# Kernel tuning notes

Hardware: AMD Instinct MI355X
Metric: run time of the kernel (lower is better)

## Reference

```python
import jax, jax.numpy as jnp
import numpy as np

D_K = 128


def setup_inputs() -> dict:
    key = jax.random.key(0)
    k1, k2, k3, k4 = jax.random.split(key, 4)
    return {
        "value_in": jax.random.normal(k1, (4, 2048, 1024), dtype=jnp.float32),
        "w_q": jax.random.normal(k2, (1024, D_K), dtype=jnp.float32),
        "w_k": jax.random.normal(k3, (1024, D_K), dtype=jnp.float32),
        "w_v": jax.random.normal(k4, (1024, 128), dtype=jnp.float32),
    }


def reference(value_in, w_q, w_k, w_v):
    # Projections: [B,S,d_model] @ [d_model,d] -> [B,S,d]
    q = jnp.einsum('bsm,mk->bsk', value_in, w_q)
    k = jnp.einsum('bsm,mk->bsk', value_in, w_k)
    v = jnp.einsum('bsm,mv->bsv', value_in, w_v)
    # Scores [B,S,S], scaled by sqrt(d_k)
    scores = jnp.einsum('bqk,bsk->bqs', q, k) / jnp.sqrt(jnp.float32(D_K))
    S = scores.shape[-1]
    # Causal mask: keep lower triangle (q_idx >= k_idx), -inf elsewhere
    causal = jnp.tril(jnp.ones((S, S), dtype=bool))
    scores = jnp.where(causal, scores, -jnp.inf)
    # NOTE: softmax over the QUERY axis (dim=-2), not the key axis
    attention = jax.nn.softmax(scores, axis=-2)
    out = jnp.einsum('bqs,bsv->bqv', attention, v)
    return out, attention
```

## Files before the change

### kernel.cpp

```cpp
#include <hip/hip_runtime.h>
#include <math.h>

constexpr int B  = 4;
constexpr int S  = 2048;
constexpr int DM = 1024;
constexpr int DK = 128;
constexpr int BS = B * S;
constexpr int NSP = 8;

static constexpr float SCALE = 0.08838834764831845f;

typedef __attribute__((ext_vector_type(8))) short bf16x8;
typedef __attribute__((ext_vector_type(4))) float f32x4;
typedef __attribute__((ext_vector_type(8))) unsigned short u16x8;

__device__ __forceinline__ unsigned short f2bf(float x) {
  unsigned u = __float_as_uint(x);
  unsigned r = (u + 0x7FFFu + ((u >> 16) & 1u)) >> 16;
  return (unsigned short)r;
}
__device__ __forceinline__ float bf2f(unsigned short h) {
  return __uint_as_float(((unsigned)h) << 16);
}

__device__ __forceinline__ void gload16(const void* g, void* l) {
  __builtin_amdgcn_global_load_lds(
      (const __attribute__((address_space(1))) void*)g,
      (__attribute__((address_space(3))) void*)l, 16, 0, 0);
}

__global__ __launch_bounds__(256) void cvt_hilo(
    const float* __restrict__ x, unsigned short* __restrict__ hi,
    unsigned short* __restrict__ lo)
{
  const size_t idx = (size_t)blockIdx.x * 256 + threadIdx.x;
  const float4 v = ((const float4*)x)[idx];
  ushort4 h, l;
  h.x = f2bf(v.x); l.x = f2bf(v.x - bf2f(h.x));
  h.y = f2bf(v.y); l.y = f2bf(v.y - bf2f(h.y));
  h.z = f2bf(v.z); l.z = f2bf(v.z - bf2f(h.z));
  h.w = f2bf(v.w); l.w = f2bf(v.w - bf2f(h.w));
  ((ushort4*)hi)[idx] = h;
  ((ushort4*)lo)[idx] = l;
}

__global__ void cvtw_kernel(const float* __restrict__ wq, const float* __restrict__ wk,
                            const float* __restrict__ wv,
                            unsigned short* __restrict__ Wth, unsigned short* __restrict__ Wtl)
{
  const int n = blockIdx.x;
  const int p = n >> 7, c = n & 127;
  const float* w = (p == 0) ? wq : (p == 1) ? wk : wv;
  for (int k = threadIdx.x; k < DM; k += 256) {
    const float x = w[(size_t)k * DK + c];
    const unsigned short h = f2bf(x);
    Wth[(size_t)n * DM + k] = h;
    Wtl[(size_t)n * DM + k] = f2bf(x - bf2f(h));
  }
}

__global__ __launch_bounds__(256) void proj_mfma(
    const unsigned short* __restrict__ Ah, const unsigned short* __restrict__ Al,
    const unsigned short* __restrict__ Wh, const unsigned short* __restrict__ Wl,
    unsigned short* __restrict__ qh, unsigned short* __restrict__ ql,
    unsigned short* __restrict__ kh, unsigned short* __restrict__ kl,
    float* __restrict__ vtmp)
{
  __shared__ unsigned short Ash[2][64 * 64];
  __shared__ unsigned short Wsh[2][64 * 64];

  const int r0 = blockIdx.x * 64;
  const int n0 = blockIdx.y * 64;
  const int t  = threadIdx.x;
  const int l  = t & 63, w = t >> 6;
  const int wm = w >> 1, wn = w & 1;
  const int fr = l & 15, kg = l >> 4;

  f32x4 acc[2][2] = {};

  for (int k0 = 0; k0 < DM; k0 += 64) {
    #pragma unroll
    for (int i = 0; i < 2; ++i) {
      const int flat = t + i * 256;
      const int row = flat >> 3, sg = flat & 7;
      const int sgs = sg ^ (row & 7);
      const size_t ga = (size_t)(r0 + row) * DM + k0 + sgs * 8;
      const size_t gw = (size_t)(n0 + row) * DM + k0 + sgs * 8;
      gload16(Ah + ga, &Ash[0][flat * 8]);
      gload16(Al + ga, &Ash[1][flat * 8]);
      gload16(Wh + gw, &Wsh[0][flat * 8]);
      gload16(Wl + gw, &Wsh[1][flat * 8]);
    }
    __syncthreads();

    #pragma unroll
    for (int kk = 0; kk < 2; ++kk) {
      bf16x8 ah[2], al[2], bh[2], bl[2];
      #pragma unroll
      for (int im = 0; im < 2; ++im) {
        const int row = wm * 32 + im * 16 + fr;
        const int off = row * 64 + ((kk * 4 + kg) ^ (row & 7)) * 8;
        ah[im] = *(const bf16x8*)&Ash[0][off];
        al[im] = *(const bf16x8*)&Ash[1][off];
      }
      #pragma unroll
      for (int in = 0; in < 2; ++in) {
        const int row = wn * 32 + in * 16 + fr;
        const int off = row * 64 + ((kk * 4 + kg) ^ (row & 7)) * 8;
        bh[in] = *(const bf16x8*)&Wsh[0][off];
        bl[in] = *(const bf16x8*)&Wsh[1][off];
      }
      #pragma unroll
      for (int im = 0; im < 2; ++im)
        #pragma unroll
        for (int in = 0; in < 2; ++in) {
          acc[im][in] = __builtin_amdgcn_mfma_f32_16x16x32_bf16(ah[im], bh[in], acc[im][in], 0, 0, 0);
          acc[im][in] = __builtin_amdgcn_mfma_f32_16x16x32_bf16(ah[im], bl[in], acc[im][in], 0, 0, 0);
          acc[im][in] = __builtin_amdgcn_mfma_f32_16x16x32_bf16(al[im], bh[in], acc[im][in], 0, 0, 0);
        }
    }
    __syncthreads();
  }

  const int crow = kg * 4;
  #pragma unroll
  for (int im = 0; im < 2; ++im)
    #pragma unroll
    for (int in = 0; in < 2; ++in) {
      const int n = n0 + wn * 32 + in * 16 + fr;
      const int p = n >> 7, c = n & 127;
      #pragma unroll
      for (int r = 0; r < 4; ++r) {
        const int m = r0 + wm * 32 + im * 16 + crow + r;
        const float val = acc[im][in][r];
        if (p == 2) {
          vtmp[(size_t)m * DK + c] = val;
        } else {
          const unsigned short h = f2bf(val);
          const unsigned short lo2 = f2bf(val - bf2f(h));
          unsigned short* hd = p ? kh : qh;
          unsigned short* ld = p ? kl : ql;
          hd[(size_t)m * DK + c] = h;
          ld[(size_t)m * DK + c] = lo2;
        }
      }
    }
}

__global__ __launch_bounds__(256) void cvtv_kernel(
    const float* __restrict__ v, unsigned short* __restrict__ vTh,
    unsigned short* __restrict__ vTl)
{
  const int s0 = blockIdx.x * 64, d0 = blockIdx.y * 64, b = blockIdx.z;
  __shared__ float Ts[64][65];
  const int t = threadIdx.x;
  const int r = t >> 4, c4 = (t & 15) * 4;
  #pragma unroll
  for (int rr = 0; rr < 4; ++rr) {
    const int sl = r + 16 * rr;
    *(float4*)&Ts[sl][c4] =
        *(const float4*)&v[((size_t)b * S + s0 + sl) * DK + d0 + c4];
  }
  __syncthreads();
  const int dl = t >> 2, sq = (t & 3) * 16;
  unsigned short hbuf[16], lbuf[16];
  #pragma unroll
  for (int j = 0; j < 16; ++j) {
    const float val = Ts[sq + j][dl];
    hbuf[j] = f2bf(val);
    lbuf[j] = f2bf(val - bf2f(hbuf[j]));
  }
  const size_t o = (size_t)b * DK * S + (size_t)(d0 + dl) * S + s0 + sq;
  #pragma unroll
  for (int half = 0; half < 2; ++half) {
    *(u16x8*)&vTh[o + half * 8] = *(u16x8*)&hbuf[half * 8];
    *(u16x8*)&vTl[o + half * 8] = *(u16x8*)&lbuf[half * 8];
  }
}

__global__ __launch_bounds__(256) void stats_mfma(
    const unsigned short* __restrict__ qh, const unsigned short* __restrict__ ql,
    const unsigned short* __restrict__ kh, const unsigned short* __restrict__ kl,
    float* __restrict__ pm, float* __restrict__ ps)
{
  const int sp = blockIdx.x, qt = blockIdx.y, b = blockIdx.z;
  if (sp > qt) return;
  const int q0 = qt * 64;

  __shared__ unsigned short Bsh[64 * 128], Bsl[64 * 128];
  __shared__ float SmL[64 * 2], SeL[64 * 2];

  const int t = threadIdx.x;
  const int l = t & 63, w = t >> 6;
  const int wm = w >> 1, wn = w & 1;
  const int fr = l & 15, kg = l >> 4;

  #pragma unroll
  for (int i = 0; i < 4; ++i) {
    const int flat = t + i * 256;
    const int row = flat >> 4, sg = flat & 15;
    const int sgs = sg ^ (row & 7);
    const size_t gq = (size_t)(b * S + q0 + row) * DK + sgs * 8;
    gload16(qh + gq, &Bsh[flat * 8]);
    gload16(ql + gq, &Bsl[flat * 8]);
  }
  __syncthreads();
  bf16x8 qfh[2][4], qfl[2][4];
  #pragma unroll
  for (int im = 0; im < 2; ++im)
    #pragma unroll
    for (int ks = 0; ks < 4; ++ks) {
      const int row = wm * 32 + im * 16 + fr;
      const int off = row * 128 + ((ks * 4 + kg) ^ (row & 7)) * 8;
      qfh[im][ks] = *(const bf16x8*)&Bsh[off];
      qfl[im][ks] = *(const bf16x8*)&Bsl[off];
    }
  __syncthreads();

  for (int st = sp; st <= qt; st += NSP) {
    const int s0 = st * 64;

    #pragma unroll
    for (int i = 0; i < 4; ++i) {
      const int flat = t + i * 256;
      const int row = flat >> 4, sg = flat & 15;
      const int sgs = sg ^ (row & 7);
      const size_t gk = (size_t)(b * S + s0 + row) * DK + sgs * 8;
      gload16(kh + gk, &Bsh[flat * 8]);
      gload16(kl + gk, &Bsl[flat * 8]);
    }
    __syncthreads();

    f32x4 acc[2][2] = {};
    #pragma unroll
    for (int ks = 0; ks < 4; ++ks) {
      bf16x8 bh[2], bl[2];
      #pragma unroll
      for (int in = 0; in < 2; ++in) {
        const int row = wn * 32 + in * 16 + fr;
        const int off = row * 128 + ((ks * 4 + kg) ^ (row & 7)) * 8;
        bh[in] = *(const bf16x8*)&Bsh[off];
        bl[in] = *(const bf16x8*)&Bsl[off];
      }
      #pragma unroll
      for (int im = 0; im < 2; ++im)
        #pragma unroll
        for (int in = 0; in < 2; ++in) {
          acc[im][in] = __builtin_amdgcn_mfma_f32_16x16x32_bf16(qfh[im][ks], bh[in], acc[im][in], 0, 0, 0);
          acc[im][in] = __builtin_amdgcn_mfma_f32_16x16x32_bf16(qfh[im][ks], bl[in], acc[im][in], 0, 0, 0);
          acc[im][in] = __builtin_amdgcn_mfma_f32_16x16x32_bf16(qfl[im][ks], bh[in], acc[im][in], 0, 0, 0);
        }
    }

    const bool diag = (st == qt);
    float Sm_[2], Se_[2];
    #pragma unroll
    for (int in = 0; in < 2; ++in) {
      const int scol = s0 + wn * 32 + in * 16 + fr;
      float m8 = -INFINITY;
      #pragma unroll
      for (int im = 0; im < 2; ++im)
        #pragma unroll
        for (int r = 0; r < 4; ++r) {
          const int q = q0 + wm * 32 + im * 16 + kg * 4 + r;
          if (!diag || q >= scol) m8 = fmaxf(m8, acc[im][in][r] * SCALE);
        }
      float e8 = 0.f;
      if (m8 > -INFINITY) {
        #pragma unroll
        for (int im = 0; im < 2; ++im)
          #pragma unroll
          for (int r = 0; r < 4; ++r) {
            const int q = q0 + wm * 32 + im * 16 + kg * 4 + r;
            if (!diag || q >= scol) e8 += __expf(acc[im][in][r] * SCALE - m8);
          }
      }
      #pragma unroll
      for (int off = 16; off <= 32; off <<= 1) {
        const float om = __shfl_xor(m8, off);
        const float oe = __shfl_xor(e8, off);
        const float nm = fmaxf(m8, om);
        float ne = 0.f;
        if (m8 > -INFINITY) ne += e8 * __expf(m8 - nm);
        if (om > -INFINITY) ne += oe * __expf(om - nm);
        m8 = nm; e8 = ne;
      }
      Sm_[in] = m8; Se_[in] = e8;
    }
    if (l < 16) {
      #pragma unroll
      for (int in = 0; in < 2; ++in) {
        const int col = wn * 32 + in * 16 + l;
        SmL[col * 2 + wm] = Sm_[in];
        SeL[col * 2 + wm] = Se_[in];
      }
    }
    __syncthreads();
    if (t < 64) {
      const float m0 = SmL[t * 2 + 0], m1 = SmL[t * 2 + 1];
      const float nm = fmaxf(m0, m1);
      float ne = 0.f;
      if (m0 > -INFINITY) ne += SeL[t * 2 + 0] * __expf(m0 - nm);
      if (m1 > -INFINITY) ne += SeL[t * 2 + 1] * __expf(m1 - nm);
      const size_t o = ((size_t)(b * 32 + qt)) * S + s0 + t;
      pm[o] = nm;
      ps[o] = ne;
    }
    __syncthreads();
  }
}

__global__ void colcombine_kernel(const float* __restrict__ pm, const float* __restrict__ ps,
                                  float* __restrict__ cm, float* __restrict__ cinv)
{
  const int s = blockIdx.x * 256 + threadIdx.x;
  const int b = blockIdx.y;
  const int ch0 = s >> 6;
  float m = -INFINITY;
  for (int ch = ch0; ch < 32; ++ch)
    m = fmaxf(m, pm[((size_t)(b * 32 + ch)) * S + s]);
  float sum = 0.f;
  for (int ch = ch0; ch < 32; ++ch) {
    const size_t i = ((size_t)(b * 32 + ch)) * S + s;
    sum += ps[i] * __expf(pm[i] - m);
  }
  cm[(size_t)b * S + s]   = m;
  cinv[(size_t)b * S + s] = 1.f / sum;
}

__global__ void zero_out_kernel(float* __restrict__ out)
{
  const size_t idx = (size_t)blockIdx.x * 256 + threadIdx.x;
  ((float4*)out)[idx] = float4{0.f, 0.f, 0.f, 0.f};
}

__global__ __launch_bounds__(256) void fused_pv(
    const unsigned short* __restrict__ qh, const unsigned short* __restrict__ ql,
    const unsigned short* __restrict__ kh, const unsigned short* __restrict__ kl,
    const unsigned short* __restrict__ vTh, const unsigned short* __restrict__ vTl,
    const float* __restrict__ cm, const float* __restrict__ cinv,
    float* __restrict__ att, float* __restrict__ out)
{
  const int sp = blockIdx.x, qt = blockIdx.y, b = blockIdx.z;
  if (sp > qt) return;
  const int q0 = qt * 64;
  float* attb = att + (size_t)b * S * S;
  const unsigned short* vth = vTh + (size_t)b * DK * S;
  const unsigned short* vtl = vTl + (size_t)b * DK * S;

  __shared__ unsigned short Ksh[64 * 128], Ksl[64 * 128];
  __shared__ unsigned short Vsh[128 * 64], Vsl[128 * 64];
  __shared__ unsigned short Psh[64 * 64];

  const int t = threadIdx.x;
  const int l = t & 63, w = t >> 6;
  const int wm = w >> 1, wn = w & 1;
  const int fr = l & 15, kg = l >> 4;

  #pragma unroll
  for (int i = 0; i < 4; ++i) {
    const int flat = t + i * 256;
    const int row = flat >> 4, sg = flat & 15;
    const int sgs = sg ^ (row & 7);
    const size_t gq = (size_t)(b * S + q0 + row) * DK + sgs * 8;
    gload16(qh + gq, &Ksh[flat * 8]);
    gload16(ql + gq, &Ksl[flat * 8]);
  }
  __syncthreads();
  bf16x8 qfh[2][4], qfl[2][4];
  #pragma unroll
  for (int im = 0; im < 2; ++im)
    #pragma unroll
    for (int ks = 0; ks < 4; ++ks) {
      const int row = wm * 32 + im * 16 + fr;
      const int off = row * 128 + ((ks * 4 + kg) ^ (row & 7)) * 8;
      qfh[im][ks] = *(const bf16x8*)&Ksh[off];
      qfl[im][ks] = *(const bf16x8*)&Ksl[off];
    }
  __syncthreads();

  f32x4 acc[8] = {};

  for (int st = sp; st <= qt; st += NSP) {
    const int s0 = st * 64;

    #pragma unroll
    for (int i = 0; i < 4; ++i) {
      const int flat = t + i * 256;
      const int row = flat >> 4, sg = flat & 15;
      const int sgs = sg ^ (row & 7);
      const size_t gk = (size_t)(b * S + s0 + row) * DK + sgs * 8;
      gload16(kh + gk, &Ksh[flat * 8]);
      gload16(kl + gk, &Ksl[flat * 8]);
    }
    #pragma unroll
    for (int i = 0; i < 4; ++i) {
      const int flat = t + i * 256;
      const int row = flat >> 3, sg = flat & 7;
      const int sgs = sg ^ (row & 7);
      const size_t gv = (size_t)row * S + s0 + sgs * 8;
      gload16(vth + gv, &Vsh[flat * 8]);
      gload16(vtl + gv, &Vsl[flat * 8]);
    }
    __syncthreads();

    f32x4 sacc[2][2] = {};
    #pragma unroll
    for (int ks = 0; ks < 4; ++ks) {
      bf16x8 bh[2], bl[2];
      #pragma unroll
      for (int in = 0; in < 2; ++in) {
        const int row = wn * 32 + in * 16 + fr;
        const int off = row * 128 + ((ks * 4 + kg) ^ (row & 7)) * 8;
        bh[in] = *(const bf16x8*)&Ksh[off];
        bl[in] = *(const bf16x8*)&Ksl[off];
      }
      #pragma unroll
      for (int im = 0; im < 2; ++im)
        #pragma unroll
        for (int in = 0; in < 2; ++in) {
          sacc[im][in] = __builtin_amdgcn_mfma_f32_16x16x32_bf16(qfh[im][ks], bh[in], sacc[im][in], 0, 0, 0);
          sacc[im][in] = __builtin_amdgcn_mfma_f32_16x16x32_bf16(qfh[im][ks], bl[in], sacc[im][in], 0, 0, 0);
          sacc[im][in] = __builtin_amdgcn_mfma_f32_16x16x32_bf16(qfl[im][ks], bh[in], sacc[im][in], 0, 0, 0);
        }
    }

    const bool diag = (st == qt);
    float xv[2][2][4];
    #pragma unroll
    for (int in = 0; in < 2; ++in) {
      const int sloc = wn * 32 + in * 16 + fr;
      const int scol = s0 + sloc;
      const float m   = cm[(size_t)b * S + scol];
      const float inv = cinv[(size_t)b * S + scol];
      #pragma unroll
      for (int im = 0; im < 2; ++im) {
        #pragma unroll
        for (int r = 0; r < 4; ++r) {
          const int qloc = wm * 32 + im * 16 + kg * 4 + r;
          const bool live = !diag || (q0 + qloc >= scol);
          const float x = live ? __expf(sacc[im][in][r] * SCALE - m) * inv : 0.f;
          xv[im][in][r] = x;
          const int idx = qloc * 64 + (((sloc >> 3) ^ (qloc & 7)) * 8 + (sloc & 7));
          Psh[idx] = f2bf(x);
        }
      }
    }

    if (st < qt) {
      const f32x4 z = {0.f, 0.f, 0.f, 0.f};
      #pragma unroll
      for (int i = 0; i < 4; ++i) {
        const int flat = t + i * 256;
        const int row = flat >> 4, c4 = (flat & 15) * 4;
        __builtin_nontemporal_store(z, (f32x4*)&attb[(size_t)(s0 + row) * S + q0 + c4]);
      }
    }

    #pragma unroll
    for (int im = 0; im < 2; ++im)
      #pragma unroll
      for (int in = 0; in < 2; ++in) {
        const int sloc = wn * 32 + in * 16 + fr;
        #pragma unroll
        for (int r = 0; r < 4; ++r) {
          const int qloc = wm * 32 + im * 16 + kg * 4 + r;
          __builtin_nontemporal_store(xv[im][in][r],
                                      &attb[(size_t)(q0 + qloc) * S + s0 + sloc]);
        }
      }
    __syncthreads();

    #pragma unroll
    for (int ks2 = 0; ks2 < 2; ++ks2) {
      const int arow = w * 16 + fr;
      const int aoff = arow * 64 + ((ks2 * 4 + kg) ^ (arow & 7)) * 8;
      const bf16x8 a = *(const bf16x8*)&Psh[aoff];
      #pragma unroll
      for (int in = 0; in < 8; ++in) {
        const int brow = in * 16 + fr;
        const int boff = brow * 64 + ((ks2 * 4 + kg) ^ (brow & 7)) * 8;
        const bf16x8 b_h = *(const bf16x8*)&Vsh[boff];
        const bf16x8 b_l = *(const bf16x8*)&Vsl[boff];
        acc[in] = __builtin_amdgcn_mfma_f32_16x16x32_bf16(a, b_h, acc[in], 0, 0, 0);
        acc[in] = __builtin_amdgcn_mfma_f32_16x16x32_bf16(a, b_l, acc[in], 0, 0, 0);
      }
    }
    __syncthreads();
  }

  #pragma unroll
  for (int in = 0; in < 8; ++in) {
    #pragma unroll
    for (int r = 0; r < 4; ++r) {
      const int q = q0 + w * 16 + kg * 4 + r;
      const int d = in * 16 + fr;
      atomicAdd(&out[((size_t)b * S + q) * DK + d], acc[in][r]);
    }
  }
}

extern "C" void kernel_launch(void* const* d_in, const int* in_sizes, int n_in,
                              void* d_out, int out_size, void* d_ws, size_t ws_size,
                              hipStream_t stream)
{
  const float* vin = (const float*)d_in[0];
  const float* wq  = (const float*)d_in[1];
  const float* wk  = (const float*)d_in[2];
  const float* wv  = (const float*)d_in[3];

  float* out = (float*)d_out;
  float* att = out + (size_t)B * S * DK;

  unsigned short* Ah  = (unsigned short*)att;
  unsigned short* Al  = Ah  + (size_t)BS * DM;
  unsigned short* Wth = Al  + (size_t)BS * DM;
  unsigned short* Wtl = Wth + (size_t)384 * DM;

  constexpr size_t NE = (size_t)BS * DK;
  unsigned short* qh  = (unsigned short*)d_ws;
  unsigned short* ql  = qh  + NE;
  unsigned short* kh  = ql  + NE;
  unsigned short* kl  = kh  + NE;
  unsigned short* vTh = kl  + NE;
  unsigned short* vTl = vTh + NE;
  float* vtmp = (float*)(vTl + NE);
  float* pm   = vtmp;
  float* ps   = pm + 32ull * B * S;
  float* cm   = ps + 32ull * B * S;
  float* cinv = cm + (size_t)B * S;

  cvt_hilo         <<<dim3(BS * DM / 1024),  256, 0, stream>>>(vin, Ah, Al);
  cvtw_kernel      <<<dim3(384),             256, 0, stream>>>(wq, wk, wv, Wth, Wtl);
  proj_mfma        <<<dim3(128, 6),          256, 0, stream>>>(Ah, Al, Wth, Wtl,
                                                               qh, ql, kh, kl, vtmp);
  cvtv_kernel      <<<dim3(S / 64, 2, B),    256, 0, stream>>>(vtmp, vTh, vTl);
  zero_out_kernel  <<<dim3(BS * DK / 1024),  256, 0, stream>>>(out);
  stats_mfma       <<<dim3(NSP, 32, B),      256, 0, stream>>>(qh, ql, kh, kl, pm, ps);
  colcombine_kernel<<<dim3(S / 256, B),      256, 0, stream>>>(pm, ps, cm, cinv);
  fused_pv         <<<dim3(NSP, 32, B),      256, 0, stream>>>(qh, ql, kh, kl, vTh, vTl,
                                                               cm, cinv, att, out);
}
```

Before: 117.8 us.

## Defer attention-tile stores to next iteration to overlap with K/V loads

Stores of the attention tile and its mirrored zero tile are moved from right after the softmax into the start of the next iteration. There they are issued after the next K/V global loads and before the barrier, with an epilogue that flushes the final tile. The intent is to overlap the large global write traffic with load latency and MFMA work instead of serialising it between barriers. A trailing __syncthreads in the stats kernel loop is also dropped. This keeps xv live across iterations, which raises register pressure, and relies on the removed barrier being unnecessary.

After: 115.5 us. About the same (-1.9%).

```diff
diff --git a/kernel.cpp b/kernel.cpp
--- a/kernel.cpp
+++ b/kernel.cpp
@@ -306,7 +306,6 @@
       pm[o] = nm;
       ps[o] = ne;
     }
-    __syncthreads();
   }
 }
 
@@ -380,6 +379,9 @@
   __syncthreads();
 
   f32x4 acc[8] = {};
+  float xv[2][2][4];
+  int prev_s0 = -1;
+  int prev_mirror = 0;
 
   for (int st = sp; st <= qt; st += NSP) {
     const int s0 = st * 64;
@@ -402,6 +404,30 @@
       gload16(vth + gv, &Vsh[flat * 8]);
       gload16(vtl + gv, &Vsl[flat * 8]);
     }
+
+    if (prev_s0 >= 0) {
+      if (prev_mirror) {
+        const f32x4 z = {0.f, 0.f, 0.f, 0.f};
+        #pragma unroll
+        for (int i = 0; i < 4; ++i) {
+          const int flat = t + i * 256;
+          const int row = flat >> 4, c4 = (flat & 15) * 4;
+          __builtin_nontemporal_store(z, (f32x4*)&attb[(size_t)(prev_s0 + row) * S + q0 + c4]);
+        }
+      }
+      #pragma unroll
+      for (int im = 0; im < 2; ++im)
+        #pragma unroll
+        for (int in = 0; in < 2; ++in) {
+          const int sloc = wn * 32 + in * 16 + fr;
+          #pragma unroll
+          for (int r = 0; r < 4; ++r) {
+            const int qloc = wm * 32 + im * 16 + kg * 4 + r;
+            __builtin_nontemporal_store(xv[im][in][r],
+                                        &attb[(size_t)(q0 + qloc) * S + prev_s0 + sloc]);
+          }
+        }
+    }
     __syncthreads();
 
     f32x4 sacc[2][2] = {};
@@ -426,7 +452,6 @@
     }
 
     const bool diag = (st == qt);
-    float xv[2][2][4];
     #pragma unroll
     for (int in = 0; in < 2; ++in) {
       const int sloc = wn * 32 + in * 16 + fr;
@@ -446,29 +471,6 @@
         }
       }
     }
-
-    if (st < qt) {
-      const f32x4 z = {0.f, 0.f, 0.f, 0.f};
-      #pragma unroll
-      for (int i = 0; i < 4; ++i) {
-        const int flat = t + i * 256;
-        const int row = flat >> 4, c4 = (flat & 15) * 4;
-        __builtin_nontemporal_store(z, (f32x4*)&attb[(size_t)(s0 + row) * S + q0 + c4]);
-      }
-    }
-
-    #pragma unroll
-    for (int im = 0; im < 2; ++im)
-      #pragma unroll
-      for (int in = 0; in < 2; ++in) {
-        const int sloc = wn * 32 + in * 16 + fr;
-        #pragma unroll
-        for (int r = 0; r < 4; ++r) {
-          const int qloc = wm * 32 + im * 16 + kg * 4 + r;
-          __builtin_nontemporal_store(xv[im][in][r],
-                                      &attb[(size_t)(q0 + qloc) * S + s0 + sloc]);
-        }
-      }
     __syncthreads();
 
     #pragma unroll
@@ -487,6 +489,33 @@
       }
     }
     __syncthreads();
+
+    prev_s0 = s0;
+    prev_mirror = (st < qt) ? 1 : 0;
+  }
+
+  if (prev_s0 >= 0) {
+    if (prev_mirror) {
+      const f32x4 z = {0.f, 0.f, 0.f, 0.f};
+      #pragma unroll
+      for (int i = 0; i < 4; ++i) {
+        const int flat = t + i * 256;
+        const int row = flat >> 4, c4 = (flat & 15) * 4;
+        __builtin_nontemporal_store(z, (f32x4*)&attb[(size_t)(prev_s0 + row) * S + q0 + c4]);
+      }
+    }
+    #pragma unroll
+    for (int im = 0; im < 2; ++im)
+      #pragma unroll
+      for (int in = 0; in < 2; ++in) {
+        const int sloc = wn * 32 + in * 16 + fr;
+        #pragma unroll
+        for (int r = 0; r < 4; ++r) {
+          const int qloc = wm * 32 + im * 16 + kg * 4 + r;
+          __builtin_nontemporal_store(xv[im][in][r],
+                                      &attb[(size_t)(q0 + qloc) * S + prev_s0 + sloc]);
+        }
+      }
   }
 
   #pragma unroll
```

## Double the query tile to 128 rows with 512-thread blocks in stats and PV

Applied to the files above, without the earlier changes.

The stats and fused PV kernels now cover 128 query rows per block using 8 waves instead of 4. Each loaded K and V tile is reused across twice as many queries, which halves global and LDS traffic per output, and the partial-stat chunk count drops from 32 to 16. Attention probabilities are now stored inline as they are computed rather than buffered in registers first. The trade-offs are fewer blocks with a coarser diagonal-masking granularity, higher LDS use per block, and one barrier removed from the stats loop.

Measured after the change: 116.2 us. Within noise of the previous version (-1.3%).

```diff
diff --git a/kernel.cpp b/kernel.cpp
--- a/kernel.cpp
+++ b/kernel.cpp
@@ -7,6 +7,7 @@
 constexpr int DK = 128;
 constexpr int BS = B * S;
 constexpr int NSP = 8;
+constexpr int QT  = 16;
 
 static constexpr float SCALE = 0.08838834764831845f;
 
@@ -178,17 +179,18 @@
   }
 }
 
-__global__ __launch_bounds__(256) void stats_mfma(
+__global__ __launch_bounds__(512) void stats_mfma(
     const unsigned short* __restrict__ qh, const unsigned short* __restrict__ ql,
     const unsigned short* __restrict__ kh, const unsigned short* __restrict__ kl,
     float* __restrict__ pm, float* __restrict__ ps)
 {
   const int sp = blockIdx.x, qt = blockIdx.y, b = blockIdx.z;
-  if (sp > qt) return;
-  const int q0 = qt * 64;
-
-  __shared__ unsigned short Bsh[64 * 128], Bsl[64 * 128];
-  __shared__ float SmL[64 * 2], SeL[64 * 2];
+  const int stmax = 2 * qt + 1;
+  if (sp > stmax) return;
+  const int q0 = qt * 128;
+
+  __shared__ unsigned short Bsh[2][64 * 128], Bsl[2][64 * 128];
+  __shared__ float SmL[64 * 4], SeL[64 * 4];
 
   const int t = threadIdx.x;
   const int l = t & 63, w = t >> 6;
@@ -196,42 +198,49 @@
   const int fr = l & 15, kg = l >> 4;
 
   #pragma unroll
-  for (int i = 0; i < 4; ++i) {
-    const int flat = t + i * 256;
+  for (int i = 0; i < 2; ++i) {
+    const int flat = t + i * 512;
     const int row = flat >> 4, sg = flat & 15;
     const int sgs = sg ^ (row & 7);
-    const size_t gq = (size_t)(b * S + q0 + row) * DK + sgs * 8;
-    gload16(qh + gq, &Bsh[flat * 8]);
-    gload16(ql + gq, &Bsl[flat * 8]);
+    const size_t g1 = (size_t)(b * S + q0 + row) * DK + sgs * 8;
+    const size_t g2 = (size_t)(b * S + q0 + 64 + row) * DK + sgs * 8;
+    gload16(qh + g1, &Bsh[0][flat * 8]);
+    gload16(ql + g1, &Bsl[0][flat * 8]);
+    gload16(qh + g2, &Bsh[1][flat * 8]);
+    gload16(ql + g2, &Bsl[1][flat * 8]);
   }
   __syncthreads();
   bf16x8 qfh[2][4], qfl[2][4];
-  #pragma unroll
-  for (int im = 0; im < 2; ++im)
-    #pragma unroll
-    for (int ks = 0; ks < 4; ++ks) {
-      const int row = wm * 32 + im * 16 + fr;
-      const int off = row * 128 + ((ks * 4 + kg) ^ (row & 7)) * 8;
-      qfh[im][ks] = *(const bf16x8*)&Bsh[off];
-      qfl[im][ks] = *(const bf16x8*)&Bsl[off];
-    }
+  {
+    const int qbuf = (wm < 2) ? 0 : 1;
+    #pragma unroll
+    for (int im = 0; im < 2; ++im)
+      #pragma unroll
+      for (int ks = 0; ks < 4; ++ks) {
+        const int qloc = wm * 32 + im * 16 + fr;
+        const int row = qloc & 63;
+        const int off = row * 128 + ((ks * 4 + kg) ^ (row & 7)) * 8;
+        qfh[im][ks] = *(const bf16x8*)&Bsh[qbuf][off];
+        qfl[im][ks] = *(const bf16x8*)&Bsl[qbuf][off];
+      }
+  }
   __syncthreads();
 
-  for (int st = sp; st <= qt; st += NSP) {
+  for (int st = sp; st <= stmax; st += NSP) {
     const int s0 = st * 64;
 
     #pragma unroll
-    for (int i = 0; i < 4; ++i) {
-      const int flat = t + i * 256;
+    for (int i = 0; i < 2; ++i) {
+      const int flat = t + i * 512;
       const int row = flat >> 4, sg = flat & 15;
       const int sgs = sg ^ (row & 7);
       const size_t gk = (size_t)(b * S + s0 + row) * DK + sgs * 8;
-      gload16(kh + gk, &Bsh[flat * 8]);
-      gload16(kl + gk, &Bsl[flat * 8]);
-    }
-    __syncthreads();
-
-    f32x4 acc[2][2] = {};
+      gload16(kh + gk, &Bsh[0][flat * 8]);
+      gload16(kl + gk, &Bsl[0][flat * 8]);
+    }
+    __syncthreads();
+
+    f32x4 sacc[2][2] = {};
     #pragma unroll
     for (int ks = 0; ks < 4; ++ks) {
       bf16x8 bh[2], bl[2];
@@ -239,20 +248,20 @@
       for (int in = 0; in < 2; ++in) {
         const int row = wn * 32 + in * 16 + fr;
         const int off = row * 128 + ((ks * 4 + kg) ^ (row & 7)) * 8;
-        bh[in] = *(const bf16x8*)&Bsh[off];
-        bl[in] = *(const bf16x8*)&Bsl[off];
+        bh[in] = *(const bf16x8*)&Bsh[0][off];
+        bl[in] = *(const bf16x8*)&Bsl[0][off];
       }
       #pragma unroll
       for (int im = 0; im < 2; ++im)
         #pragma unroll
         for (int in = 0; in < 2; ++in) {
-          acc[im][in] = __builtin_amdgcn_mfma_f32_16x16x32_bf16(qfh[im][ks], bh[in], acc[im][in], 0, 0, 0);
-          acc[im][in] = __builtin_amdgcn_mfma_f32_16x16x32_bf16(qfh[im][ks], bl[in], acc[im][in], 0, 0, 0);
-          acc[im][in] = __builtin_amdgcn_mfma_f32_16x16x32_bf16(qfl[im][ks], bh[in], acc[im][in], 0, 0, 0);
+          sacc[im][in] = __builtin_amdgcn_mfma_f32_16x16x32_bf16(qfh[im][ks], bh[in], sacc[im][in], 0, 0, 0);
+          sacc[im][in] = __builtin_amdgcn_mfma_f32_16x16x32_bf16(qfh[im][ks], bl[in], sacc[im][in], 0, 0, 0);
+          sacc[im][in] = __builtin_amdgcn_mfma_f32_16x16x32_bf16(qfl[im][ks], bh[in], sacc[im][in], 0, 0, 0);
         }
     }
 
-    const bool diag = (st == qt);
+    const bool mm = (st >= 2 * qt);
     float Sm_[2], Se_[2];
     #pragma unroll
     for (int in = 0; in < 2; ++in) {
@@ -263,7 +272,7 @@
         #pragma unroll
         for (int r = 0; r < 4; ++r) {
           const int q = q0 + wm * 32 + im * 16 + kg * 4 + r;
-          if (!diag || q >= scol) m8 = fmaxf(m8, acc[im][in][r] * SCALE);
+          if (!mm || q >= scol) m8 = fmaxf(m8, sacc[im][in][r] * SCALE);
         }
       float e8 = 0.f;
       if (m8 > -INFINITY) {
@@ -272,7 +281,7 @@
           #pragma unroll
           for (int r = 0; r < 4; ++r) {
             const int q = q0 + wm * 32 + im * 16 + kg * 4 + r;
-            if (!diag || q >= scol) e8 += __expf(acc[im][in][r] * SCALE - m8);
+            if (!mm || q >= scol) e8 += __expf(sacc[im][in][r] * SCALE - m8);
           }
       }
       #pragma unroll
@@ -291,22 +300,25 @@
       #pragma unroll
       for (int in = 0; in < 2; ++in) {
         const int col = wn * 32 + in * 16 + l;
-        SmL[col * 2 + wm] = Sm_[in];
-        SeL[col * 2 + wm] = Se_[in];
+        SmL[col * 4 + wm] = Sm_[in];
+        SeL[col * 4 + wm] = Se_[in];
       }
     }
     __syncthreads();
     if (t < 64) {
-      const float m0 = SmL[t * 2 + 0], m1 = SmL[t * 2 + 1];
-      const float nm = fmaxf(m0, m1);
-      float ne = 0.f;
-      if (m0 > -INFINITY) ne += SeL[t * 2 + 0] * __expf(m0 - nm);
-      if (m1 > -INFINITY) ne += SeL[t * 2 + 1] * __expf(m1 - nm);
-      const size_t o = ((size_t)(b * 32 + qt)) * S + s0 + t;
-      pm[o] = nm;
-      ps[o] = ne;
-    }
-    __syncthreads();
+      float m = -INFINITY;
+      #pragma unroll
+      for (int y = 0; y < 4; ++y) m = fmaxf(m, SmL[t * 4 + y]);
+      float sum = 0.f;
+      #pragma unroll
+      for (int y = 0; y < 4; ++y) {
+        const float my = SmL[t * 4 + y];
+        if (my > -INFINITY) sum += SeL[t * 4 + y] * __expf(my - m);
+      }
+      const size_t o = ((size_t)(b * QT + qt)) * S + s0 + t;
+      pm[o] = m;
+      ps[o] = sum;
+    }
   }
 }
 
@@ -315,13 +327,13 @@
 {
   const int s = blockIdx.x * 256 + threadIdx.x;
   const int b = blockIdx.y;
-  const int ch0 = s >> 6;
+  const int ch0 = s >> 7;
   float m = -INFINITY;
-  for (int ch = ch0; ch < 32; ++ch)
-    m = fmaxf(m, pm[((size_t)(b * 32 + ch)) * S + s]);
+  for (int ch = ch0; ch < QT; ++ch)
+    m = fmaxf(m, pm[((size_t)(b * QT + ch)) * S + s]);
   float sum = 0.f;
-  for (int ch = ch0; ch < 32; ++ch) {
-    const size_t i = ((size_t)(b * 32 + ch)) * S + s;
+  for (int ch = ch0; ch < QT; ++ch) {
+    const size_t i = ((size_t)(b * QT + ch)) * S + s;
     sum += ps[i] * __expf(pm[i] - m);
   }
   cm[(size_t)b * S + s]   = m;
@@ -334,7 +346,7 @@
   ((float4*)out)[idx] = float4{0.f, 0.f, 0.f, 0.f};
 }
 
-__global__ __launch_bounds__(256) void fused_pv(
+__global__ __launch_bounds__(512) void fused_pv(
     const unsigned short* __restrict__ qh, const unsigned short* __restrict__ ql,
     const unsigned short* __restrict__ kh, const unsigned short* __restrict__ kl,
     const unsigned short* __restrict__ vTh, const unsigned short* __restrict__ vTl,
@@ -342,15 +354,16 @@
     float* __restrict__ att, float* __restrict__ out)
 {
   const int sp = blockIdx.x, qt = blockIdx.y, b = blockIdx.z;
-  if (sp > qt) return;
-  const int q0 = qt * 64;
+  const int stmax = 2 * qt + 1;
+  if (sp > stmax) return;
+  const int q0 = qt * 128;
   float* attb = att + (size_t)b * S * S;
   const unsigned short* vth = vTh + (size_t)b * DK * S;
   const unsigned short* vtl = vTl + (size_t)b * DK * S;
 
   __shared__ unsigned short Ksh[64 * 128], Ksl[64 * 128];
   __shared__ unsigned short Vsh[128 * 64], Vsl[128 * 64];
-  __shared__ unsigned short Psh[64 * 64];
+  __shared__ unsigned short Psh[128 * 64];
 
   const int t = threadIdx.x;
   const int l = t & 63, w = t >> 6;
@@ -358,35 +371,43 @@
   const int fr = l & 15, kg = l >> 4;
 
   #pragma unroll
-  for (int i = 0; i < 4; ++i) {
-    const int flat = t + i * 256;
+  for (int i = 0; i < 2; ++i) {
+    const int flat = t + i * 512;
     const int row = flat >> 4, sg = flat & 15;
     const int sgs = sg ^ (row & 7);
-    const size_t gq = (size_t)(b * S + q0 + row) * DK + sgs * 8;
-    gload16(qh + gq, &Ksh[flat * 8]);
-    gload16(ql + gq, &Ksl[flat * 8]);
+    const size_t g1 = (size_t)(b * S + q0 + row) * DK + sgs * 8;
+    const size_t g2 = (size_t)(b * S + q0 + 64 + row) * DK + sgs * 8;
+    gload16(qh + g1, &Ksh[flat * 8]);
+    gload16(ql + g1, &Ksl[flat * 8]);
+    gload16(qh + g2, &Vsh[flat * 8]);
+    gload16(ql + g2, &Vsl[flat * 8]);
   }
   __syncthreads();
   bf16x8 qfh[2][4], qfl[2][4];
-  #pragma unroll
-  for (int im = 0; im < 2; ++im)
-    #pragma unroll
-    for (int ks = 0; ks < 4; ++ks) {
-      const int row = wm * 32 + im * 16 + fr;
-      const int off = row * 128 + ((ks * 4 + kg) ^ (row & 7)) * 8;
-      qfh[im][ks] = *(const bf16x8*)&Ksh[off];
-      qfl[im][ks] = *(const bf16x8*)&Ksl[off];
-    }
+  {
+    const unsigned short* qsrc_h = (wm < 2) ? Ksh : Vsh;
+    const unsigned short* qsrc_l = (wm < 2) ? Ksl : Vsl;
+    #pragma unroll
+    for (int im = 0; im < 2; ++im)
+      #pragma unroll
+      for (int ks = 0; ks < 4; ++ks) {
+        const int qloc = wm * 32 + im * 16 + fr;
+        const int row = qloc & 63;
+        const int off = row * 128 + ((ks * 4 + kg) ^ (row & 7)) * 8;
+        qfh[im][ks] = *(const bf16x8*)&qsrc_h[off];
+        qfl[im][ks] = *(const bf16x8*)&qsrc_l[off];
+      }
+  }
   __syncthreads();
 
   f32x4 acc[8] = {};
 
-  for (int st = sp; st <= qt; st += NSP) {
+  for (int st = sp; st <= stmax; st += NSP) {
     const int s0 = st * 64;
 
     #pragma unroll
-    for (int i = 0; i < 4; ++i) {
-      const int flat = t + i * 256;
+    for (int i = 0; i < 2; ++i) {
+      const int flat = t + i * 512;
       const int row = flat >> 4, sg = flat & 15;
       const int sgs = sg ^ (row & 7);
       const size_t gk = (size_t)(b * S + s0 + row) * DK + sgs * 8;
@@ -394,8 +415,8 @@
       gload16(kl + gk, &Ksl[flat * 8]);
     }
     #pragma unroll
-    for (int i = 0; i < 4; ++i) {
-      const int flat = t + i * 256;
+    for (int i = 0; i < 2; ++i) {
+      const int flat = t + i * 512;
       const int row = flat >> 3, sg = flat & 7;
       const int sgs = sg ^ (row & 7);
       const size_t gv = (size_t)row * S + s0 + sgs * 8;
@@ -425,8 +446,7 @@
         }
     }
 
-    const bool diag = (st == qt);
-    float xv[2][2][4];
+    const bool mm = (st >= 2 * qt);
     #pragma unroll
     for (int in = 0; in < 2; ++in) {
       const int sloc = wn * 32 + in * 16 + fr;
@@ -438,37 +458,24 @@
         #pragma unroll
         for (int r = 0; r < 4; ++r) {
           const int qloc = wm * 32 + im * 16 + kg * 4 + r;
-          const bool live = !diag || (q0 + qloc >= scol);
+          const bool live = !mm || (q0 + qloc >= scol);
           const float x = live ? __expf(sacc[im][in][r] * SCALE - m) * inv : 0.f;
-          xv[im][in][r] = x;
           const int idx = qloc * 64 + (((sloc >> 3) ^ (qloc & 7)) * 8 + (sloc & 7));
           Psh[idx] = f2bf(x);
+          __builtin_nontemporal_store(x, &attb[(size_t)(q0 + qloc) * S + scol]);
         }
       }
     }
 
-    if (st < qt) {
+    if (st < 2 * qt) {
       const f32x4 z = {0.f, 0.f, 0.f, 0.f};
       #pragma unroll
       for (int i = 0; i < 4; ++i) {
-        const int flat = t + i * 256;
-        const int row = flat >> 4, c4 = (flat & 15) * 4;
+        const int flat = t + i * 512;
+        const int row = flat >> 5, c4 = (flat & 31) * 4;
         __builtin_nontemporal_store(z, (f32x4*)&attb[(size_t)(s0 + row) * S + q0 + c4]);
       }
     }
-
-    #pragma unroll
-    for (int im = 0; im < 2; ++im)
-      #pragma unroll
-      for (int in = 0; in < 2; ++in) {
-        const int sloc = wn * 32 + in * 16 + fr;
-        #pragma unroll
-        for (int r = 0; r < 4; ++r) {
-          const int qloc = wm * 32 + im * 16 + kg * 4 + r;
-          __builtin_nontemporal_store(xv[im][in][r],
-                                      &attb[(size_t)(q0 + qloc) * S + s0 + sloc]);
-        }
-      }
     __syncthreads();
 
     #pragma unroll
@@ -526,8 +533,8 @@
   unsigned short* vTl = vTh + NE;
   float* vtmp = (float*)(vTl + NE);
   float* pm   = vtmp;
-  float* ps   = pm + 32ull * B * S;
-  float* cm   = ps + 32ull * B * S;
+  float* ps   = pm + (size_t)QT * B * S;
+  float* cm   = ps + (size_t)QT * B * S;
   float* cinv = cm + (size_t)B * S;
 
   cvt_hilo         <<<dim3(BS * DM / 1024),  256, 0, stream>>>(vin, Ah, Al);
@@ -536,8 +543,8 @@
                                                                qh, ql, kh, kl, vtmp);
   cvtv_kernel      <<<dim3(S / 64, 2, B),    256, 0, stream>>>(vtmp, vTh, vTl);
   zero_out_kernel  <<<dim3(BS * DK / 1024),  256, 0, stream>>>(out);
-  stats_mfma       <<<dim3(NSP, 32, B),      256, 0, stream>>>(qh, ql, kh, kl, pm, ps);
+  stats_mfma       <<<dim3(NSP, QT, B),      512, 0, stream>>>(qh, ql, kh, kl, pm, ps);
   colcombine_kernel<<<dim3(S / 256, B),      256, 0, stream>>>(pm, ps, cm, cinv);
-  fused_pv         <<<dim3(NSP, 32, B),      256, 0, stream>>>(qh, ql, kh, kl, vTh, vTl,
+  fused_pv         <<<dim3(NSP, QT, B),      512, 0, stream>>>(qh, ql, kh, kl, vTh, vTl,
                                                                cm, cinv, att, out);
 }
```

## Stash unnormalized exp tiles in attention buffer to skip QK recompute

Applied to the files above, without the earlier changes.

The stats kernel now computes each tile's column max first, then exponentiates the scores and writes the unnormalized probabilities as bf16 into the masked (transposed) region of the attention output, which serves as scratch. The PV kernel no longer loads Q/K or recomputes QK^T with three MFMAs per product. Instead it reads the stashed bf16 tile, rescales it with a per-column correction built from the partial and global max and the inverse sum, writes the attention values, and then zeroes the scratch region. This trades the matmul recompute for extra global traffic and an extra LDS pass. Attention values are now rounded to bf16 precision rather than kept at fp32, which risks accuracy.

Result: slower. 120.2 us (+2.0%).

```diff
diff --git a/kernel.cpp b/kernel.cpp
--- a/kernel.cpp
+++ b/kernel.cpp
@@ -181,13 +181,15 @@
 __global__ __launch_bounds__(256) void stats_mfma(
     const unsigned short* __restrict__ qh, const unsigned short* __restrict__ ql,
     const unsigned short* __restrict__ kh, const unsigned short* __restrict__ kl,
-    float* __restrict__ pm, float* __restrict__ ps)
+    float* __restrict__ pm, float* __restrict__ ps, float* __restrict__ att)
 {
   const int sp = blockIdx.x, qt = blockIdx.y, b = blockIdx.z;
   if (sp > qt) return;
   const int q0 = qt * 64;
+  float* attb = att + (size_t)b * S * S;
 
   __shared__ unsigned short Bsh[64 * 128], Bsl[64 * 128];
+  __shared__ unsigned short Psh[64 * 64];
   __shared__ float SmL[64 * 2], SeL[64 * 2];
 
   const int t = threadIdx.x;
@@ -231,7 +233,7 @@
     }
     __syncthreads();
 
-    f32x4 acc[2][2] = {};
+    f32x4 sacc[2][2] = {};
     #pragma unroll
     for (int ks = 0; ks < 4; ++ks) {
       bf16x8 bh[2], bl[2];
@@ -246,14 +248,14 @@
       for (int im = 0; im < 2; ++im)
         #pragma unroll
         for (int in = 0; in < 2; ++in) {
-          acc[im][in] = __builtin_amdgcn_mfma_f32_16x16x32_bf16(qfh[im][ks], bh[in], acc[im][in], 0, 0, 0);
-          acc[im][in] = __builtin_amdgcn_mfma_f32_16x16x32_bf16(qfh[im][ks], bl[in], acc[im][in], 0, 0, 0);
-          acc[im][in] = __builtin_amdgcn_mfma_f32_16x16x32_bf16(qfl[im][ks], bh[in], acc[im][in], 0, 0, 0);
+          sacc[im][in] = __builtin_amdgcn_mfma_f32_16x16x32_bf16(qfh[im][ks], bh[in], sacc[im][in], 0, 0, 0);
+          sacc[im][in] = __builtin_amdgcn_mfma_f32_16x16x32_bf16(qfh[im][ks], bl[in], sacc[im][in], 0, 0, 0);
+          sacc[im][in] = __builtin_amdgcn_mfma_f32_16x16x32_bf16(qfl[im][ks], bh[in], sacc[im][in], 0, 0, 0);
         }
     }
 
     const bool diag = (st == qt);
-    float Sm_[2], Se_[2];
+    float mloc[2];
     #pragma unroll
     for (int in = 0; in < 2; ++in) {
       const int scol = s0 + wn * 32 + in * 16 + fr;
@@ -263,50 +265,58 @@
         #pragma unroll
         for (int r = 0; r < 4; ++r) {
           const int q = q0 + wm * 32 + im * 16 + kg * 4 + r;
-          if (!diag || q >= scol) m8 = fmaxf(m8, acc[im][in][r] * SCALE);
+          if (!diag || q >= scol) m8 = fmaxf(m8, sacc[im][in][r] * SCALE);
         }
+      m8 = fmaxf(m8, __shfl_xor(m8, 16));
+      m8 = fmaxf(m8, __shfl_xor(m8, 32));
+      mloc[in] = m8;
+    }
+    if (l < 16) {
+      #pragma unroll
+      for (int in = 0; in < 2; ++in)
+        SmL[(wn * 32 + in * 16 + l) * 2 + wm] = mloc[in];
+    }
+    __syncthreads();
+
+    #pragma unroll
+    for (int in = 0; in < 2; ++in) {
+      const int sloc = wn * 32 + in * 16 + fr;
+      const int scol = s0 + sloc;
+      const float m_c = fmaxf(SmL[sloc * 2 + 0], SmL[sloc * 2 + 1]);
       float e8 = 0.f;
-      if (m8 > -INFINITY) {
+      #pragma unroll
+      for (int im = 0; im < 2; ++im)
         #pragma unroll
-        for (int im = 0; im < 2; ++im)
-          #pragma unroll
-          for (int r = 0; r < 4; ++r) {
-            const int q = q0 + wm * 32 + im * 16 + kg * 4 + r;
-            if (!diag || q >= scol) e8 += __expf(acc[im][in][r] * SCALE - m8);
-          }
-      }
-      #pragma unroll
-      for (int off = 16; off <= 32; off <<= 1) {
-        const float om = __shfl_xor(m8, off);
-        const float oe = __shfl_xor(e8, off);
-        const float nm = fmaxf(m8, om);
-        float ne = 0.f;
-        if (m8 > -INFINITY) ne += e8 * __expf(m8 - nm);
-        if (om > -INFINITY) ne += oe * __expf(om - nm);
-        m8 = nm; e8 = ne;
-      }
-      Sm_[in] = m8; Se_[in] = e8;
-    }
-    if (l < 16) {
-      #pragma unroll
-      for (int in = 0; in < 2; ++in) {
-        const int col = wn * 32 + in * 16 + l;
-        SmL[col * 2 + wm] = Sm_[in];
-        SeL[col * 2 + wm] = Se_[in];
-      }
-    }
-    __syncthreads();
+        for (int r = 0; r < 4; ++r) {
+          const int qloc = wm * 32 + im * 16 + kg * 4 + r;
+          const bool live = !diag || (q0 + qloc >= scol);
+          const float x = live ? __expf(sacc[im][in][r] * SCALE - m_c) : 0.f;
+          e8 += x;
+          const int idx = qloc * 64 + (((sloc >> 3) ^ (qloc & 7)) * 8 + (sloc & 7));
+          Psh[idx] = f2bf(x);
+        }
+      e8 += __shfl_xor(e8, 16);
+      e8 += __shfl_xor(e8, 32);
+      if (l < 16) SeL[sloc * 2 + wm] = e8;
+    }
+    __syncthreads();
+
     if (t < 64) {
-      const float m0 = SmL[t * 2 + 0], m1 = SmL[t * 2 + 1];
-      const float nm = fmaxf(m0, m1);
-      float ne = 0.f;
-      if (m0 > -INFINITY) ne += SeL[t * 2 + 0] * __expf(m0 - nm);
-      if (m1 > -INFINITY) ne += SeL[t * 2 + 1] * __expf(m1 - nm);
+      const float m_c = fmaxf(SmL[t * 2 + 0], SmL[t * 2 + 1]);
+      const float sum = SeL[t * 2 + 0] + SeL[t * 2 + 1];
       const size_t o = ((size_t)(b * 32 + qt)) * S + s0 + t;
-      pm[o] = nm;
-      ps[o] = ne;
-    }
-    __syncthreads();
+      pm[o] = m_c;
+      ps[o] = sum;
+    }
+
+    {
+      const int q  = t >> 2;
+      const int co = (t & 3) * 16;
+      unsigned short* dst = (unsigned short*)attb;
+      const size_t o = ((size_t)(s0 + q) * S + q0) * 2 + co;
+      *(u16x8*)&dst[o + 0] = *(const u16x8*)&Psh[q * 64 + co + 0];
+      *(u16x8*)&dst[o + 8] = *(const u16x8*)&Psh[q * 64 + co + 8];
+    }
   }
 }
 
@@ -335,10 +345,9 @@
 }
 
 __global__ __launch_bounds__(256) void fused_pv(
-    const unsigned short* __restrict__ qh, const unsigned short* __restrict__ ql,
-    const unsigned short* __restrict__ kh, const unsigned short* __restrict__ kl,
     const unsigned short* __restrict__ vTh, const unsigned short* __restrict__ vTl,
-    const float* __restrict__ cm, const float* __restrict__ cinv,
+    const float* __restrict__ pm, const float* __restrict__ cm,
+    const float* __restrict__ cinv,
     float* __restrict__ att, float* __restrict__ out)
 {
   const int sp = blockIdx.x, qt = blockIdx.y, b = blockIdx.z;
@@ -348,36 +357,14 @@
   const unsigned short* vth = vTh + (size_t)b * DK * S;
   const unsigned short* vtl = vTl + (size_t)b * DK * S;
 
-  __shared__ unsigned short Ksh[64 * 128], Ksl[64 * 128];
   __shared__ unsigned short Vsh[128 * 64], Vsl[128 * 64];
   __shared__ unsigned short Psh[64 * 64];
+  __shared__ float corrL[64];
 
   const int t = threadIdx.x;
   const int l = t & 63, w = t >> 6;
-  const int wm = w >> 1, wn = w & 1;
   const int fr = l & 15, kg = l >> 4;
-
-  #pragma unroll
-  for (int i = 0; i < 4; ++i) {
-    const int flat = t + i * 256;
-    const int row = flat >> 4, sg = flat & 15;
-    const int sgs = sg ^ (row & 7);
-    const size_t gq = (size_t)(b * S + q0 + row) * DK + sgs * 8;
-    gload16(qh + gq, &Ksh[flat * 8]);
-    gload16(ql + gq, &Ksl[flat * 8]);
-  }
-  __syncthreads();
-  bf16x8 qfh[2][4], qfl[2][4];
-  #pragma unroll
-  for (int im = 0; im < 2; ++im)
-    #pragma unroll
-    for (int ks = 0; ks < 4; ++ks) {
-      const int row = wm * 32 + im * 16 + fr;
-      const int off = row * 128 + ((ks * 4 + kg) ^ (row & 7)) * 8;
-      qfh[im][ks] = *(const bf16x8*)&Ksh[off];
-      qfl[im][ks] = *(const bf16x8*)&Ksl[off];
-    }
-  __syncthreads();
+  const int nr = t >> 4, c4 = (t & 15) * 4;
 
   f32x4 acc[8] = {};
 
@@ -385,13 +372,12 @@
     const int s0 = st * 64;
 
     #pragma unroll
-    for (int i = 0; i < 4; ++i) {
+    for (int i = 0; i < 2; ++i) {
       const int flat = t + i * 256;
-      const int row = flat >> 4, sg = flat & 15;
-      const int sgs = sg ^ (row & 7);
-      const size_t gk = (size_t)(b * S + s0 + row) * DK + sgs * 8;
-      gload16(kh + gk, &Ksh[flat * 8]);
-      gload16(kl + gk, &Ksl[flat * 8]);
+      const int q = flat >> 3, sg = flat & 7;
+      const unsigned short* src =
+          (const unsigned short*)attb + ((size_t)(s0 + q) * S + q0) * 2 + sg * 8;
+      gload16(src, &Psh[flat * 8]);
     }
     #pragma unroll
     for (int i = 0; i < 4; ++i) {
@@ -402,49 +388,37 @@
       gload16(vth + gv, &Vsh[flat * 8]);
       gload16(vtl + gv, &Vsl[flat * 8]);
     }
-    __syncthreads();
-
-    f32x4 sacc[2][2] = {};
-    #pragma unroll
-    for (int ks = 0; ks < 4; ++ks) {
-      bf16x8 bh[2], bl[2];
-      #pragma unroll
-      for (int in = 0; in < 2; ++in) {
-        const int row = wn * 32 + in * 16 + fr;
-        const int off = row * 128 + ((ks * 4 + kg) ^ (row & 7)) * 8;
-        bh[in] = *(const bf16x8*)&Ksh[off];
-        bl[in] = *(const bf16x8*)&Ksl[off];
-      }
-      #pragma unroll
-      for (int im = 0; im < 2; ++im)
-        #pragma unroll
-        for (int in = 0; in < 2; ++in) {
-          sacc[im][in] = __builtin_amdgcn_mfma_f32_16x16x32_bf16(qfh[im][ks], bh[in], sacc[im][in], 0, 0, 0);
-          sacc[im][in] = __builtin_amdgcn_mfma_f32_16x16x32_bf16(qfh[im][ks], bl[in], sacc[im][in], 0, 0, 0);
-          sacc[im][in] = __builtin_amdgcn_mfma_f32_16x16x32_bf16(qfl[im][ks], bh[in], sacc[im][in], 0, 0, 0);
-        }
-    }
-
-    const bool diag = (st == qt);
-    float xv[2][2][4];
-    #pragma unroll
-    for (int in = 0; in < 2; ++in) {
-      const int sloc = wn * 32 + in * 16 + fr;
-      const int scol = s0 + sloc;
-      const float m   = cm[(size_t)b * S + scol];
-      const float inv = cinv[(size_t)b * S + scol];
-      #pragma unroll
-      for (int im = 0; im < 2; ++im) {
-        #pragma unroll
-        for (int r = 0; r < 4; ++r) {
-          const int qloc = wm * 32 + im * 16 + kg * 4 + r;
-          const bool live = !diag || (q0 + qloc >= scol);
-          const float x = live ? __expf(sacc[im][in][r] * SCALE - m) * inv : 0.f;
-          xv[im][in][r] = x;
-          const int idx = qloc * 64 + (((sloc >> 3) ^ (qloc & 7)) * 8 + (sloc & 7));
-          Psh[idx] = f2bf(x);
-        }
-      }
+    if (t < 64) {
+      const int s = s0 + t;
+      const float pmv = pm[((size_t)(b * 32 + qt)) * S + s];
+      corrL[t] = __expf(pmv - cm[(size_t)b * S + s]) * cinv[(size_t)b * S + s];
+    }
+    __syncthreads();
+
+    {
+      const int base = t * 16;
+      #pragma unroll
+      for (int u = 0; u < 16; ++u) {
+        const int j = base + u;
+        const int q = j >> 6;
+        const int grp = (j >> 3) & 7;
+        const int sl = ((grp ^ (q & 7)) << 3) | (j & 7);
+        Psh[j] = f2bf(bf2f(Psh[j]) * corrL[sl]);
+      }
+    }
+    __syncthreads();
+
+    #pragma unroll
+    for (int rr = 0; rr < 4; ++rr) {
+      const int qloc = nr + 16 * rr;
+      const int idx = qloc * 64 + (((c4 >> 3) ^ (qloc & 7)) * 8 + (c4 & 7));
+      float4 x;
+      x.x = bf2f(Psh[idx + 0]);
+      x.y = bf2f(Psh[idx + 1]);
+      x.z = bf2f(Psh[idx + 2]);
+      x.w = bf2f(Psh[idx + 3]);
+      __builtin_nontemporal_store(*(f32x4*)&x,
+          (f32x4*)&attb[(size_t)(q0 + qloc) * S + s0 + c4]);
     }
 
     if (st < qt) {
@@ -452,24 +426,10 @@
       #pragma unroll
       for (int i = 0; i < 4; ++i) {
         const int flat = t + i * 256;
-        const int row = flat >> 4, c4 = (flat & 15) * 4;
-        __builtin_nontemporal_store(z, (f32x4*)&attb[(size_t)(s0 + row) * S + q0 + c4]);
-      }
-    }
-
-    #pragma unroll
-    for (int im = 0; im < 2; ++im)
-      #pragma unroll
-      for (int in = 0; in < 2; ++in) {
-        const int sloc = wn * 32 + in * 16 + fr;
-        #pragma unroll
-        for (int r = 0; r < 4; ++r) {
-          const int qloc = wm * 32 + im * 16 + kg * 4 + r;
-          __builtin_nontemporal_store(xv[im][in][r],
-                                      &attb[(size_t)(q0 + qloc) * S + s0 + sloc]);
-        }
-      }
-    __syncthreads();
+        const int row = flat >> 4, cc = (flat & 15) * 4;
+        __builtin_nontemporal_store(z, (f32x4*)&attb[(size_t)(s0 + row) * S + q0 + cc]);
+      }
+    }
 
     #pragma unroll
     for (int ks2 = 0; ks2 < 2; ++ks2) {
@@ -536,8 +496,8 @@
                                                                qh, ql, kh, kl, vtmp);
   cvtv_kernel      <<<dim3(S / 64, 2, B),    256, 0, stream>>>(vtmp, vTh, vTl);
   zero_out_kernel  <<<dim3(BS * DK / 1024),  256, 0, stream>>>(out);
-  stats_mfma       <<<dim3(NSP, 32, B),      256, 0, stream>>>(qh, ql, kh, kl, pm, ps);
+  stats_mfma       <<<dim3(NSP, 32, B),      256, 0, stream>>>(qh, ql, kh, kl, pm, ps, att);
   colcombine_kernel<<<dim3(S / 256, B),      256, 0, stream>>>(pm, ps, cm, cinv);
-  fused_pv         <<<dim3(NSP, 32, B),      256, 0, stream>>>(qh, ql, kh, kl, vTh, vTl,
-                                                               cm, cinv, att, out);
-}
+  fused_pv         <<<dim3(NSP, 32, B),      256, 0, stream>>>(vTh, vTl, pm, cm, cinv,
+                                                               att, out);
+}
```
